# Kernel tuning notes

Hardware: AMD Instinct MI355X
Metric: run time of the kernel (lower is better)

## Reference

```python
import jax, jax.numpy as jnp
import numpy as np

B, S, V = 512, 256, 10      # batch, s_node_num, v_node_num
E, H = 128, 128             # embedding, lstm hidden
D = 2 * H                   # num_directions * hidden
PENALTY = 1.0e6
STD = 0.1


def _cell(x, h, c, Wih, Whh, b):
    # PyTorch LSTM cell, gate order i, f, g, o; b = b_ih + b_hh
    g = x @ Wih.T + h @ Whh.T + b
    i, f, gg, o = jnp.split(g, 4, axis=-1)
    c = jax.nn.sigmoid(f) * c + jax.nn.sigmoid(i) * jnp.tanh(gg)
    h = jax.nn.sigmoid(o) * jnp.tanh(c)
    return h, c


def setup_inputs() -> dict:
    key = jax.random.key(0)
    ks = jax.random.split(key, 25)
    w = lambda k, shp: (jax.random.normal(k, shp, jnp.float32) * STD)
    return {
        's_node_indexes': jax.random.randint(ks[0], (B, S), 0, S, dtype=jnp.int32),
        's_inputs': jax.random.uniform(ks[1], (B, S, 3), jnp.float32),
        'v_input': jax.random.uniform(ks[2], (V, 3), jnp.float32) * 0.5,
        'W_embed': w(ks[3], (E, 1)),
        'enc_Wih_f': w(ks[4], (4 * H, E)), 'enc_Whh_f': w(ks[5], (4 * H, H)), 'enc_b_f': w(ks[6], (4 * H,)),
        'enc_Wih_b': w(ks[7], (4 * H, E)), 'enc_Whh_b': w(ks[8], (4 * H, H)), 'enc_b_b': w(ks[9], (4 * H,)),
        'dec_Wih_f': w(ks[10], (4 * H, D)), 'dec_Whh_f': w(ks[11], (4 * H, H)), 'dec_b_f': w(ks[12], (4 * H,)),
        'dec_Wih_b': w(ks[13], (4 * H, D)), 'dec_Whh_b': w(ks[14], (4 * H, H)), 'dec_b_b': w(ks[15], (4 * H,)),
        'W_ref': w(ks[16], (D, D)), 'W_q': w(ks[17], (D, D)), 'v_w': w(ks[18], (D,)),
        'W_ref2': w(ks[19], (D, D)), 'W_q2': w(ks[20], (D, D)), 'v2_w': w(ks[21], (D,)),
    }


def reference(s_node_indexes, s_inputs, v_input, W_embed,
              enc_Wih_f, enc_Whh_f, enc_b_f, enc_Wih_b, enc_Whh_b, enc_b_b,
              dec_Wih_f, dec_Whh_f, dec_b_f, dec_Wih_b, dec_Whh_b, dec_b_b,
              W_ref, W_q, v_w, W_ref2, W_q2, v2_w):
    Bn, Sn = s_node_indexes.shape
    # Embed: snode resource -> Linear(1, E, bias=False)
    emb = s_inputs[:, :, 0:1] @ W_embed.T            # (B, S, E)
    xs = jnp.swapaxes(emb, 0, 1)                     # (S, B, E)
    h0 = jnp.zeros((Bn, H), jnp.float32)
    c0 = jnp.zeros((Bn, H), jnp.float32)

    def enc_scan(Wih, Whh, b, seq):
        def step(carry, x):
            h, c = carry
            h, c = _cell(x, h, c, Wih, Whh, b)
            return (h, c), h
        (hT, cT), hs = jax.lax.scan(step, (h0, c0), seq)
        return hs, hT, cT

    hs_f, hf, cf = enc_scan(enc_Wih_f, enc_Whh_f, enc_b_f, xs)
    hs_b, hb, cb = enc_scan(enc_Wih_b, enc_Whh_b, enc_b_b, xs[::-1])
    Enc = jnp.swapaxes(jnp.concatenate([hs_f, hs_b[::-1]], axis=-1), 0, 1)  # (B, S, D)
    h_state = jnp.stack([hf, hb])                    # (2, B, H)
    c_state = jnp.stack([cf, cb])

    refE = Enc @ W_ref.T                             # (B, S, D) precomputed (dropout p=0)
    ref2E = Enc @ W_ref2.T

    def dec_step(carry, vcpu):
        dec_in, h, c, played = carry                 # dec_in (B, D)
        hf_, cf_ = _cell(dec_in, h[0], c[0], dec_Wih_f, dec_Whh_f, dec_b_f)
        hb_, cb_ = _cell(dec_in, h[1], c[1], dec_Wih_b, dec_Whh_b, dec_b_b)
        dec_out = jnp.concatenate([hf_, hb_], axis=-1)                       # (B, D)
        cannot = (s_inputs[:, :, 0] < vcpu).astype(jnp.float32) + played     # (B, S)
        ow = jnp.tanh(refE + (dec_out @ W_q.T)[:, None, :]) @ v_w - PENALTY * cannot
        att = jax.nn.softmax(jnp.tanh(ref2E + (dec_in @ W_q2.T)[:, None, :]) @ v2_w, axis=1)
        new_in = jnp.einsum('bs,bsd->bd', att, Enc)
        sel = jnp.argmax(ow, axis=1)
        played = played + jax.nn.one_hot(sel, Sn, dtype=jnp.float32)
        return (new_in, jnp.stack([hf_, hb_]), jnp.stack([cf_, cb_]), played), (ow, sel)

    init = (jnp.zeros((Bn, D), jnp.float32), h_state, c_state, jnp.zeros((Bn, Sn), jnp.float32))
    _, (output_weights, sels) = jax.lax.scan(dec_step, init, v_input[:, 0])
    shuffled = sels.T                                # (B, V)
    original = jnp.take_along_axis(s_node_indexes, shuffled, axis=1)
    return original, shuffled, output_weights        # output_weights: (V, B, S)
```

## Files before the change

### kernel.cpp

```cpp
#include <hip/hip_runtime.h>
#include <math.h>

#define cB 512
#define cS 256
#define cV 10
#define cE 128
#define cH 128
#define cD 256
#define cG 512
#define PEN 1.0e6f
#define S1 224
#define PADK 40

typedef _Float16 half8_t __attribute__((ext_vector_type(8)));
typedef _Float16 half4_t __attribute__((ext_vector_type(4)));
typedef float f32x4 __attribute__((ext_vector_type(4)));

#define DOT4(acc, wv, hv)                                   \
    do {                                                    \
        acc = fmaf((wv).x, (hv).x, acc);                    \
        acc = fmaf((wv).y, (hv).y, acc);                    \
        acc = fmaf((wv).z, (hv).z, acc);                    \
        acc = fmaf((wv).w, (hv).w, acc);                    \
    } while (0)

__device__ __forceinline__ float sigmf(float x) { return 1.0f / (1.0f + expf(-x)); }

__global__ void k_uprep(const float* __restrict__ Wih_f, const float* __restrict__ Wih_b,
                        const float* __restrict__ W_embed, float* __restrict__ uvec)
{
    const int j = threadIdx.x;
    const float* __restrict__ Wih = blockIdx.x ? Wih_b : Wih_f;
    float u = 0.f;
#pragma unroll 8
    for (int e = 0; e < cE; ++e) u = fmaf(Wih[(size_t)j * cE + e], W_embed[e], u);
    uvec[blockIdx.x * cG + j] = u;
}

__global__ __launch_bounds__(1024, 4) void k_encoder(
    const float* __restrict__ s_inputs, const float* __restrict__ uvec,
    const float* __restrict__ Whh_f, const float* __restrict__ b_f,
    const float* __restrict__ Whh_b, const float* __restrict__ b_b,
    _Float16* __restrict__ Ehi, _Float16* __restrict__ Elo,
    float* __restrict__ h_state, float* __restrict__ c_state)
{
    const int dir = blockIdx.x >> 7;
    const int b0  = (blockIdx.x & 127) * 4;
    const float* __restrict__ Whh = dir ? Whh_b : Whh_f;
    const float* __restrict__ bv  = dir ? b_b   : b_f;
    const int tid = threadIdx.x;
    const int j = tid & 511;
    const int hf = tid >> 9;

    __shared__ __align__(16) float a_in[4][cS];
    __shared__ __align__(16) float hbuf[4][cH];
    __shared__ __align__(16) float gpart[4][2][516];

    a_in[tid >> 8][tid & 255] =
        s_inputs[((size_t)(b0 + (tid >> 8)) * cS + (tid & 255)) * 3];

    float4 w[16];
#pragma unroll
    for (int kk = 0; kk < 16; ++kk)
        w[kk] = *(const float4*)&Whh[(size_t)j * cH + hf * 64 + kk * 4];

    const float uj = (hf == 0) ? uvec[dir * cG + j] : 0.f;
    const float bj = (hf == 0) ? bv[j] : 0.f;

    const int ur = tid >> 7, uk = tid & 127;
    float c_reg = 0.f, h_last = 0.f;
    if (tid < 512) hbuf[ur][uk] = 0.f;
    __syncthreads();

    for (int p = 0; p < cS; ++p) {
        const int s = dir ? (cS - 1 - p) : p;
        float acc0 = fmaf(a_in[0][s], uj, bj);
        float acc1 = fmaf(a_in[1][s], uj, bj);
        float acc2 = fmaf(a_in[2][s], uj, bj);
        float acc3 = fmaf(a_in[3][s], uj, bj);
#pragma unroll
        for (int kk = 0; kk < 16; ++kk) {
            const float4 wv = w[kk];
            const float4 h0 = *(const float4*)&hbuf[0][hf * 64 + kk * 4];
            DOT4(acc0, wv, h0);
            const float4 h1 = *(const float4*)&hbuf[1][hf * 64 + kk * 4];
            DOT4(acc1, wv, h1);
            const float4 h2 = *(const float4*)&hbuf[2][hf * 64 + kk * 4];
            DOT4(acc2, wv, h2);
            const float4 h3 = *(const float4*)&hbuf[3][hf * 64 + kk * 4];
            DOT4(acc3, wv, h3);
        }
        gpart[0][hf][j] = acc0;
        gpart[1][hf][j] = acc1;
        gpart[2][hf][j] = acc2;
        gpart[3][hf][j] = acc3;
        __syncthreads();

        if (tid < 512) {
            const float gi = gpart[ur][0][uk]       + gpart[ur][1][uk];
            const float gf = gpart[ur][0][128 + uk] + gpart[ur][1][128 + uk];
            const float gg = gpart[ur][0][256 + uk] + gpart[ur][1][256 + uk];
            const float go = gpart[ur][0][384 + uk] + gpart[ur][1][384 + uk];
            const float i_ = sigmf(gi), f_ = sigmf(gf), g_ = tanhf(gg), o_ = sigmf(go);
            c_reg = fmaf(f_, c_reg, i_ * g_);
            const float hn = o_ * tanhf(c_reg);
            h_last = hn;
            hbuf[ur][uk] = hn;
            const size_t eidx = ((size_t)(b0 + ur) * cS + s) * cD + dir * cH + uk;
            const _Float16 hh = (_Float16)hn;
            Ehi[eidx] = hh;
            Elo[eidx] = (_Float16)(hn - (float)hh);
        }
        __syncthreads();
    }
    if (tid < 512) {
        h_state[((size_t)dir * cB + b0 + ur) * cH + uk] = h_last;
        c_state[((size_t)dir * cB + b0 + ur) * cH + uk] = c_reg;
    }
}

__global__ void k_split_w(const float* __restrict__ W1, const float* __restrict__ W2,
                          _Float16* __restrict__ Whi1, _Float16* __restrict__ Wlo1,
                          _Float16* __restrict__ Whi2, _Float16* __restrict__ Wlo2)
{
    const int i = blockIdx.x * 256 + threadIdx.x;
    {
        float a = W1[i]; _Float16 h = (_Float16)a;
        Whi1[i] = h; Wlo1[i] = (_Float16)(a - (float)h);
    }
    {
        float a = W2[i]; _Float16 h = (_Float16)a;
        Whi2[i] = h; Wlo2[i] = (_Float16)(a - (float)h);
    }
}

__global__ __launch_bounds__(256) void k_head_mat(
    const _Float16* __restrict__ Ahi, const _Float16* __restrict__ Alo,
    const _Float16* __restrict__ Whi, const _Float16* __restrict__ Wlo,
    float* __restrict__ outv)
{
    const int tid = threadIdx.x;
    const int w = tid >> 6, l = tid & 63;
    const int m0 = blockIdx.x * 64;

    __shared__ __align__(16) _Float16 As[2][64][PADK];
    __shared__ __align__(16) _Float16 Ws[2][256][PADK];

    const int r = tid >> 2, kq = tid & 3;
    size_t arow;
    {
        const int m = m0 + r;
        const int s = m >> 9, b = m & 511;
        arow = ((size_t)b * cS + s) * cD;
    }
    const size_t wrow = (size_t)tid * cD;

    f32x4 acc[16];
#pragma unroll
    for (int i = 0; i < 16; ++i) acc[i] = (f32x4){0.f, 0.f, 0.f, 0.f};

    const int fr = w * 16 + (l & 15);
    const int kc = (l >> 4) * 8;

    for (int k0 = 0; k0 < 256; k0 += 32) {
        __syncthreads();
        *(uint4*)&As[0][r][kq * 8] = *(const uint4*)&Ahi[arow + k0 + kq * 8];
        *(uint4*)&As[1][r][kq * 8] = *(const uint4*)&Alo[arow + k0 + kq * 8];
#pragma unroll
        for (int q4 = 0; q4 < 4; ++q4) {
            *(uint4*)&Ws[0][tid][q4 * 8] = *(const uint4*)&Whi[wrow + k0 + q4 * 8];
            *(uint4*)&Ws[1][tid][q4 * 8] = *(const uint4*)&Wlo[wrow + k0 + q4 * 8];
        }
        __syncthreads();

        const half8_t ahi = *(const half8_t*)&As[0][fr][kc];
        const half8_t alo = *(const half8_t*)&As[1][fr][kc];
#pragma unroll
        for (int nf = 0; nf < 16; ++nf) {
            const int n = nf * 16 + (l & 15);
            const half8_t bhi = *(const half8_t*)&Ws[0][n][kc];
            const half8_t blo = *(const half8_t*)&Ws[1][n][kc];
            acc[nf] = __builtin_amdgcn_mfma_f32_16x16x32_f16(ahi, bhi, acc[nf], 0, 0, 0);
            acc[nf] = __builtin_amdgcn_mfma_f32_16x16x32_f16(ahi, blo, acc[nf], 0, 0, 0);
            acc[nf] = __builtin_amdgcn_mfma_f32_16x16x32_f16(alo, bhi, acc[nf], 0, 0, 0);
        }
    }
#pragma unroll
    for (int nf = 0; nf < 16; ++nf)
#pragma unroll
        for (int rr = 0; rr < 4; ++rr) {
            const int m = w * 16 + ((l >> 4) << 2) + rr;
            outv[(size_t)(m0 + m) * cD + nf * 16 + (l & 15)] = acc[nf][rr];
        }
}

template <int MODE>
__global__ __launch_bounds__(512, 2) void k_head2(
    const _Float16* __restrict__ Ahi, const _Float16* __restrict__ Alo,
    const _Float16* __restrict__ Whi, const _Float16* __restrict__ Wlo,
    const float* __restrict__ qv, const float* __restrict__ vv,
    float* __restrict__ outv)
{
    const int tid = threadIdx.x;
    const int l = tid & 63;
    const int w = tid >> 6;
    const int wm = w >> 2, wn = w & 3;
    const int g = l >> 4, li = l & 15;
    const int m0 = blockIdx.x * 128;

    __shared__ __align__(16) _Float16 Ah[128][PADK];
    __shared__ __align__(16) _Float16 Al[128][PADK];
    __shared__ __align__(16) _Float16 Wh[256][PADK];
    __shared__ __align__(16) _Float16 Wl[256][PADK];
    __shared__ __align__(16) float qs[4][cD];
    __shared__ __align__(16) float vs[cD];
    __shared__ float spart[4][128];

    if (MODE == 0) {
        const int b = m0 >> 8;
        if (tid < 256) qs[0][tid] = qv[(size_t)b * cD + tid];
        else           vs[tid - 256] = vv[tid - 256];
    } else {
        const int b0 = m0 >> 5;
        qs[tid >> 8][tid & 255] = qv[(size_t)(b0 + (tid >> 8)) * cD + (tid & 255)];
        const int i2 = tid + 512;
        qs[i2 >> 8][i2 & 255] = qv[(size_t)(b0 + (i2 >> 8)) * cD + (i2 & 255)];
        if (tid < 256) vs[tid] = vv[tid];
    }

    const int ar = tid >> 2, aq = tid & 3;
    size_t arow;
    {
        const int m = m0 + ar;
        if (MODE == 0) arow = (size_t)m * cD;
        else { const int b = m >> 5, s = S1 + (m & 31); arow = ((size_t)b * cS + s) * cD; }
    }

    f32x4 acc[4][4];
#pragma unroll
    for (int mi = 0; mi < 4; ++mi)
#pragma unroll
        for (int ni = 0; ni < 4; ++ni) acc[mi][ni] = (f32x4){0.f, 0.f, 0.f, 0.f};

    for (int k0 = 0; k0 < 256; k0 += 32) {
        __syncthreads();
        *(uint4*)&Ah[ar][aq * 8] = *(const uint4*)&Ahi[arow + k0 + aq * 8];
        *(uint4*)&Al[ar][aq * 8] = *(const uint4*)&Alo[arow + k0 + aq * 8];
        *(uint4*)&Wh[ar][aq * 8] = *(const uint4*)&Whi[(size_t)ar * cD + k0 + aq * 8];
        *(uint4*)&Wl[ar][aq * 8] = *(const uint4*)&Wlo[(size_t)ar * cD + k0 + aq * 8];
        *(uint4*)&Wh[ar + 128][aq * 8] = *(const uint4*)&Whi[(size_t)(ar + 128) * cD + k0 + aq * 8];
        *(uint4*)&Wl[ar + 128][aq * 8] = *(const uint4*)&Wlo[(size_t)(ar + 128) * cD + k0 + aq * 8];
        __syncthreads();

        half8_t ah[4], al[4];
#pragma unroll
        for (int mi = 0; mi < 4; ++mi) {
            ah[mi] = *(const half8_t*)&Ah[wm * 64 + mi * 16 + li][g * 8];
            al[mi] = *(const half8_t*)&Al[wm * 64 + mi * 16 + li][g * 8];
        }
#pragma unroll
        for (int ni = 0; ni < 4; ++ni) {
            const half8_t bh = *(const half8_t*)&Wh[wn * 64 + ni * 16 + li][g * 8];
            const half8_t bl = *(const half8_t*)&Wl[wn * 64 + ni * 16 + li][g * 8];
#pragma unroll
            for (int mi = 0; mi < 4; ++mi) {
                acc[mi][ni] = __builtin_amdgcn_mfma_f32_16x16x32_f16(ah[mi], bh, acc[mi][ni], 0, 0, 0);
                acc[mi][ni] = __builtin_amdgcn_mfma_f32_16x16x32_f16(ah[mi], bl, acc[mi][ni], 0, 0, 0);
                acc[mi][ni] = __builtin_amdgcn_mfma_f32_16x16x32_f16(al[mi], bh, acc[mi][ni], 0, 0, 0);
            }
        }
    }

    float val = 0.f;
#pragma unroll
    for (int mi = 0; mi < 4; ++mi)
#pragma unroll
        for (int rr = 0; rr < 4; ++rr) {
            const int row = wm * 64 + mi * 16 + g * 4 + rr;
            const int bl = (MODE == 1) ? (row >> 5) : 0;
            float p = 0.f;
#pragma unroll
            for (int ni = 0; ni < 4; ++ni) {
                const int c = wn * 64 + ni * 16 + li;
                p = fmaf(vs[c], tanhf(acc[mi][ni][rr] + qs[bl][c]), p);
            }
            p += __shfl_xor(p, 1);
            p += __shfl_xor(p, 2);
            p += __shfl_xor(p, 4);
            p += __shfl_xor(p, 8);
            if (li == mi * 4 + rr) val = p;
        }
    {
        const int row_out = wm * 64 + (li >> 2) * 16 + g * 4 + (li & 3);
        spart[wn][row_out] = val;
    }
    __syncthreads();
    if (tid < 128)
        outv[m0 + tid] = spart[0][tid] + spart[1][tid] + spart[2][tid] + spart[3][tid];
}

__global__ __launch_bounds__(256, 4) void k_fold(
    const float* __restrict__ refC, const float* __restrict__ q1v,
    const float* __restrict__ v_w, float* __restrict__ sc1lo)
{
    const int tid = threadIdx.x;
    const int m0 = blockIdx.x * 64;
    const int r = tid >> 2, p = tid & 3;
    const int m = m0 + r;
    const int b = m & 511;
    __shared__ float red[64][4];

    const float* row  = refC + (size_t)m * cD + p * 64;
    const float* qrow = q1v + (size_t)b * cD + p * 64;
    const float* vrow = v_w + p * 64;
    float s = 0.f;
#pragma unroll 4
    for (int d = 0; d < 64; d += 4) {
        const float4 rv4 = *(const float4*)&row[d];
        const float4 q4  = *(const float4*)&qrow[d];
        const float4 v4  = *(const float4*)&vrow[d];
        s = fmaf(v4.x, tanhf(rv4.x + q4.x), s);
        s = fmaf(v4.y, tanhf(rv4.y + q4.y), s);
        s = fmaf(v4.z, tanhf(rv4.z + q4.z), s);
        s = fmaf(v4.w, tanhf(rv4.w + q4.w), s);
    }
    red[r][p] = s;
    __syncthreads();
    if (tid < 64)
        sc1lo[m0 + tid] = red[tid][0] + red[tid][1] + red[tid][2] + red[tid][3];
}

__global__ __launch_bounds__(512, 2) void k_dec_cells(
    const float* __restrict__ dec_in,
    const float* __restrict__ Wih_f, const float* __restrict__ Whh_f, const float* __restrict__ b_f,
    const float* __restrict__ Wih_b, const float* __restrict__ Whh_b, const float* __restrict__ b_b,
    float* __restrict__ h_state, float* __restrict__ c_state, float* __restrict__ dec_out)
{
    const int cell = blockIdx.x >> 7;
    const int b0 = (blockIdx.x & 127) * 4;
    const float* __restrict__ Wih = cell ? Wih_b : Wih_f;
    const float* __restrict__ Whh = cell ? Whh_b : Whh_f;
    const float* __restrict__ bv  = cell ? b_b   : b_f;
    const int j = threadIdx.x;

    __shared__ __align__(16) float xin[4][cD];
    __shared__ __align__(16) float hin[4][cH];
    __shared__ __align__(16) float gbuf[4][cG];

    for (int idx = j; idx < 4 * cD; idx += 512) {
        int bb = idx >> 8, k = idx & 255;
        xin[bb][k] = dec_in[(size_t)(b0 + bb) * cD + k];
    }
    {
        int bb = j >> 7, k = j & 127;
        hin[bb][k] = h_state[((size_t)cell * cB + b0 + bb) * cH + k];
    }
    __syncthreads();

    float a0 = bv[j];
    float a1 = a0, a2 = a0, a3 = a0;
#pragma unroll 4
    for (int kk = 0; kk < 64; ++kk) {
        const float4 wv = *(const float4*)&Wih[(size_t)j * cD + kk * 4];
        const float4 x0 = *(const float4*)&xin[0][kk * 4]; DOT4(a0, wv, x0);
        const float4 x1 = *(const float4*)&xin[1][kk * 4]; DOT4(a1, wv, x1);
        const float4 x2 = *(const float4*)&xin[2][kk * 4]; DOT4(a2, wv, x2);
        const float4 x3 = *(const float4*)&xin[3][kk * 4]; DOT4(a3, wv, x3);
    }
#pragma unroll 4
    for (int kk = 0; kk < 32; ++kk) {
        const float4 wv = *(const float4*)&Whh[(size_t)j * cH + kk * 4];
        const float4 h0 = *(const float4*)&hin[0][kk * 4]; DOT4(a0, wv, h0);
        const float4 h1 = *(const float4*)&hin[1][kk * 4]; DOT4(a1, wv, h1);
        const float4 h2 = *(const float4*)&hin[2][kk * 4]; DOT4(a2, wv, h2);
        const float4 h3 = *(const float4*)&hin[3][kk * 4]; DOT4(a3, wv, h3);
    }
    gbuf[0][j] = a0; gbuf[1][j] = a1; gbuf[2][j] = a2; gbuf[3][j] = a3;
    __syncthreads();

    const int uk = j & 127, ub = j >> 7;
    const float gi = gbuf[ub][uk];
    const float gf = gbuf[ub][128 + uk];
    const float gg = gbuf[ub][256 + uk];
    const float go = gbuf[ub][384 + uk];
    const size_t sidx = ((size_t)cell * cB + b0 + ub) * cH + uk;
    const float c_old = c_state[sidx];
    const float i_ = sigmf(gi), f_ = sigmf(gf), g_ = tanhf(gg), o_ = sigmf(go);
    const float cn = fmaf(f_, c_old, i_ * g_);
    const float hn = o_ * tanhf(cn);
    c_state[sidx] = cn;
    h_state[sidx] = hn;
    dec_out[(size_t)(b0 + ub) * cD + cell * cH + uk] = hn;
}

__global__ __launch_bounds__(256, 2) void k_qproj(
    const float* __restrict__ dec_out, const float* __restrict__ dec_in_old,
    const float* __restrict__ W_q, const float* __restrict__ W_q2,
    float* __restrict__ q1v, float* __restrict__ q2v)
{
    const int b = blockIdx.x;
    const int tid = threadIdx.x;
    __shared__ __align__(16) float dout[cD];
    __shared__ __align__(16) float din[cD];
    dout[tid] = dec_out[(size_t)b * cD + tid];
    din[tid]  = dec_in_old[(size_t)b * cD + tid];
    __syncthreads();
    float s1 = 0.0f, s2 = 0.0f;
#pragma unroll 4
    for (int kk = 0; kk < 64; ++kk) {
        const float4 w1 = *(const float4*)&W_q[(size_t)tid * cD + kk * 4];
        const float4 w2 = *(const float4*)&W_q2[(size_t)tid * cD + kk * 4];
        const float4 x1 = *(const float4*)&dout[kk * 4];
        const float4 x2 = *(const float4*)&din[kk * 4];
        DOT4(s1, w1, x1);
        DOT4(s2, w2, x2);
    }
    q1v[(size_t)b * cD + tid] = s1;
    q2v[(size_t)b * cD + tid] = s2;
}

__global__ __launch_bounds__(256, 2) void k_finish(
    const float* __restrict__ sc1lo, const float* __restrict__ sc1hi,
    const float* __restrict__ sc2,
    const _Float16* __restrict__ Ehi, const _Float16* __restrict__ Elo,
    const float* __restrict__ s_inputs, const int* __restrict__ s_node_indexes,
    const float* __restrict__ v_input, float* __restrict__ played,
    float* __restrict__ dec_in_new, float* __restrict__ outp, int t)
{
    const int b = blockIdx.x;
    const int tid = threadIdx.x;
    const int lane = tid & 63;
    const int wv = tid >> 6;

    __shared__ __align__(16) float atr[cS];
    __shared__ __align__(16) float part[4][cD];
    __shared__ float rv[cS];
    __shared__ int   ri[cS];

    const float owv = (tid < S1) ? sc1lo[(size_t)tid * cB + b]
                                 : sc1hi[(size_t)b * (cS - S1) + (tid - S1)];
    atr[tid] = sc2[(size_t)b * cS + tid];

    const float vcpu = v_input[t * 3];
    float val;
    {
        const float a0 = s_inputs[((size_t)b * cS + tid) * 3];
        const float can = (a0 < vcpu ? 1.0f : 0.0f) + played[(size_t)b * cS + tid];
        val = owv - PEN * can;
        outp[2 * cB * cV + ((size_t)t * cB + b) * cS + tid] = val;
    }
    rv[tid] = val; ri[tid] = tid;
    __syncthreads();
#pragma unroll
    for (int off = 128; off > 0; off >>= 1) {
        if (tid < off) {
            const float v2 = rv[tid + off]; const int i2 = ri[tid + off];
            const float v1 = rv[tid];       const int i1 = ri[tid];
            if (v2 > v1 || (v2 == v1 && i2 < i1)) { rv[tid] = v2; ri[tid] = i2; }
        }
        __syncthreads();
    }
    const int sel = ri[0];
    __syncthreads();
    if (tid == 0) {
        played[(size_t)b * cS + sel] += 1.0f;
        outp[(size_t)b * cV + t] = (float)s_node_indexes[(size_t)b * cS + sel];
        outp[(size_t)cB * cV + (size_t)b * cV + t] = (float)sel;
    }

    rv[tid] = atr[tid];
    __syncthreads();
#pragma unroll
    for (int off = 128; off > 0; off >>= 1) {
        if (tid < off) { const float v2 = rv[tid + off]; if (v2 > rv[tid]) rv[tid] = v2; }
        __syncthreads();
    }
    const float mx = rv[0];
    __syncthreads();
    const float ex = expf(atr[tid] - mx);
    rv[tid] = ex;
    __syncthreads();
#pragma unroll
    for (int off = 128; off > 0; off >>= 1) {
        if (tid < off) rv[tid] += rv[tid + off];
        __syncthreads();
    }
    const float ssum = rv[0];
    __syncthreads();
    atr[tid] = ex / ssum;
    __syncthreads();

    {
        float4 acc = make_float4(0.f, 0.f, 0.f, 0.f);
        for (int s2i = wv * 64; s2i < wv * 64 + 64; ++s2i) {
            const float a = atr[s2i];
            const size_t eidx = ((size_t)b * cS + s2i) * cD + lane * 4;
            const half4_t h4 = *(const half4_t*)&Ehi[eidx];
            const half4_t l4 = *(const half4_t*)&Elo[eidx];
            acc.x = fmaf(a, (float)h4[0] + (float)l4[0], acc.x);
            acc.y = fmaf(a, (float)h4[1] + (float)l4[1], acc.y);
            acc.z = fmaf(a, (float)h4[2] + (float)l4[2], acc.z);
            acc.w = fmaf(a, (float)h4[3] + (float)l4[3], acc.w);
        }
        *(float4*)&part[wv][lane * 4] = acc;
    }
    __syncthreads();
    dec_in_new[(size_t)b * cD + tid] =
        part[0][tid] + part[1][tid] + part[2][tid] + part[3][tid];
}

extern "C" void kernel_launch(void* const* d_in, const int* in_sizes, int n_in,
                              void* d_out, int out_size, void* d_ws, size_t ws_size,
                              hipStream_t stream)
{
    (void)in_sizes; (void)n_in; (void)out_size; (void)ws_size;

    const int*   s_node = (const int*)  d_in[0];
    const float* s_inp  = (const float*)d_in[1];
    const float* v_inp  = (const float*)d_in[2];
    const float* W_emb  = (const float*)d_in[3];
    const float* eWih_f = (const float*)d_in[4];
    const float* eWhh_f = (const float*)d_in[5];
    const float* eb_f   = (const float*)d_in[6];
    const float* eWih_b = (const float*)d_in[7];
    const float* eWhh_b = (const float*)d_in[8];
    const float* eb_b   = (const float*)d_in[9];
    const float* dWih_f = (const float*)d_in[10];
    const float* dWhh_f = (const float*)d_in[11];
    const float* db_f   = (const float*)d_in[12];
    const float* dWih_b = (const float*)d_in[13];
    const float* dWhh_b = (const float*)d_in[14];
    const float* db_b   = (const float*)d_in[15];
    const float* W_ref  = (const float*)d_in[16];
    const float* W_q    = (const float*)d_in[17];
    const float* v_w    = (const float*)d_in[18];
    const float* W_ref2 = (const float*)d_in[19];
    const float* W_q2   = (const float*)d_in[20];
    const float* v2_w   = (const float*)d_in[21];

    float* out = (float*)d_out;
    const size_t ENCSZ = (size_t)cB * cS * cD;
    const size_t SMALL = (size_t)cB * cD;

    char* p = (char*)d_ws;
    _Float16* Ehi = (_Float16*)p; p += ENCSZ * 2;
    _Float16* Elo = (_Float16*)p; p += ENCSZ * 2;
    float* refC  = (float*)p;     p += (size_t)S1 * cB * cD * 4;
    _Float16* Whi1 = (_Float16*)p; p += (size_t)cD * cD * 2;
    _Float16* Wlo1 = (_Float16*)p; p += (size_t)cD * cD * 2;
    _Float16* Whi2 = (_Float16*)p; p += (size_t)cD * cD * 2;
    _Float16* Wlo2 = (_Float16*)p; p += (size_t)cD * cD * 2;
    float* hst    = (float*)p; p += SMALL * 4;
    float* cst    = (float*)p; p += SMALL * 4;
    float* din0   = (float*)p; p += SMALL * 4;
    float* din1   = (float*)p; p += SMALL * 4;
    float* doutb  = (float*)p; p += SMALL * 4;
    float* played = (float*)p; p += SMALL * 4;
    float* q1v    = (float*)p; p += SMALL * 4;
    float* q2v    = (float*)p; p += SMALL * 4;
    float* sc2    = (float*)p; p += SMALL * 4;
    float* sc1lo  = (float*)p; p += (size_t)S1 * cB * 4;
    float* sc1hi  = (float*)p; p += (size_t)(cS - S1) * cB * 4;
    float* uvec   = (float*)p; p += 2 * cG * 4;

    hipMemsetAsync(played, 0, SMALL * sizeof(float), stream);
    hipMemsetAsync(din0,   0, SMALL * sizeof(float), stream);

    k_split_w<<<256, 256, 0, stream>>>(W_ref, W_ref2, Whi1, Wlo1, Whi2, Wlo2);
    k_uprep<<<2, 512, 0, stream>>>(eWih_f, eWih_b, W_emb, uvec);

    k_encoder<<<256, 1024, 0, stream>>>(s_inp, uvec, eWhh_f, eb_f, eWhh_b, eb_b,
                                        Ehi, Elo, hst, cst);

    k_head_mat<<<(S1 * cB) / 64, 256, 0, stream>>>(Ehi, Elo, Whi1, Wlo1, refC);

    for (int t = 0; t < cV; ++t) {
        float* di_old = (t & 1) ? din1 : din0;
        float* di_new = (t & 1) ? din0 : din1;
        k_dec_cells<<<256, 512, 0, stream>>>(di_old, dWih_f, dWhh_f, db_f,
                                             dWih_b, dWhh_b, db_b, hst, cst, doutb);
        k_qproj<<<512, 256, 0, stream>>>(doutb, di_old, W_q, W_q2, q1v, q2v);
        k_head2<0><<<(cB * cS) / 128, 512, 0, stream>>>(Ehi, Elo, Whi2, Wlo2,
                                                        q2v, v2_w, sc2);
        k_head2<1><<<(cB * (cS - S1)) / 128, 512, 0, stream>>>(Ehi, Elo, Whi1, Wlo1,
                                                               q1v, v_w, sc1hi);
        k_fold<<<(S1 * cB) / 64, 256, 0, stream>>>(refC, q1v, v_w, sc1lo);

        k_finish<<<512, 256, 0, stream>>>(sc1lo, sc1hi, sc2, Ehi, Elo,
                                          s_inp, s_node, v_inp, played, di_new, out, t);
    }
}
```

Baseline: 3.468 ms.

## Rebalance precomputed-vs-recomputed attention projections across both heads

Instead of caching W_ref·Enc for the first 224 positions and recomputing the rest plus the full W_ref2 projection every decoder step, both heads now cache part of their projection once (112 positions for the pointer head, 128 for the glimpse head). The remaining positions are recomputed per step with MFMA stripe kernels. The cached parts are folded with tanh/dot in one combined kernel. This trades per-step MFMA recompute of the attention head against extra fp32 cache traffic, and adds a second one-time projection GEMM plus more workspace. The encoder inner loop is also rewritten into unrolled array form with no change in behaviour.

```diff
diff --git a/kernel.cpp b/kernel.cpp
--- a/kernel.cpp
+++ b/kernel.cpp
@@ -9,8 +9,11 @@
 #define cD 256
 #define cG 512
 #define PEN 1.0e6f
-#define S1 224
 #define PADK 40
+#define S1OW 112
+#define L1OW 144
+#define S2AT 128
+#define L2AT 128
 
 typedef _Float16 half8_t __attribute__((ext_vector_type(8)));
 typedef _Float16 half4_t __attribute__((ext_vector_type(4)));
@@ -74,26 +77,20 @@
 
     for (int p = 0; p < cS; ++p) {
         const int s = dir ? (cS - 1 - p) : p;
-        float acc0 = fmaf(a_in[0][s], uj, bj);
-        float acc1 = fmaf(a_in[1][s], uj, bj);
-        float acc2 = fmaf(a_in[2][s], uj, bj);
-        float acc3 = fmaf(a_in[3][s], uj, bj);
+        float a0[4];
+#pragma unroll
+        for (int r = 0; r < 4; ++r) a0[r] = fmaf(a_in[r][s], uj, bj);
 #pragma unroll
         for (int kk = 0; kk < 16; ++kk) {
             const float4 wv = w[kk];
-            const float4 h0 = *(const float4*)&hbuf[0][hf * 64 + kk * 4];
-            DOT4(acc0, wv, h0);
-            const float4 h1 = *(const float4*)&hbuf[1][hf * 64 + kk * 4];
-            DOT4(acc1, wv, h1);
-            const float4 h2 = *(const float4*)&hbuf[2][hf * 64 + kk * 4];
-            DOT4(acc2, wv, h2);
-            const float4 h3 = *(const float4*)&hbuf[3][hf * 64 + kk * 4];
-            DOT4(acc3, wv, h3);
-        }
-        gpart[0][hf][j] = acc0;
-        gpart[1][hf][j] = acc1;
-        gpart[2][hf][j] = acc2;
-        gpart[3][hf][j] = acc3;
+#pragma unroll
+            for (int r = 0; r < 4; ++r) {
+                const float4 h4 = *(const float4*)&hbuf[r][hf * 64 + kk * 4];
+                DOT4(a0[r], wv, h4);
+            }
+        }
+#pragma unroll
+        for (int r = 0; r < 4; ++r) gpart[r][hf][j] = a0[r];
         __syncthreads();
 
         if (tid < 512) {
@@ -194,8 +191,96 @@
         }
 }
 
-template <int MODE>
-__global__ __launch_bounds__(512, 2) void k_head2(
+__global__ __launch_bounds__(512, 2) void k_stripe_att(
+    const _Float16* __restrict__ Ahi, const _Float16* __restrict__ Alo,
+    const _Float16* __restrict__ Whi, const _Float16* __restrict__ Wlo,
+    const float* __restrict__ qv, const float* __restrict__ vv,
+    float* __restrict__ outv)
+{
+    const int tid = threadIdx.x;
+    const int l = tid & 63;
+    const int w = tid >> 6;
+    const int wm = w >> 2, wn = w & 3;
+    const int g = l >> 4, li = l & 15;
+    const int b = blockIdx.x;
+
+    __shared__ __align__(16) _Float16 Ah[128][PADK];
+    __shared__ __align__(16) _Float16 Al[128][PADK];
+    __shared__ __align__(16) _Float16 Wh[256][PADK];
+    __shared__ __align__(16) _Float16 Wl[256][PADK];
+    __shared__ __align__(16) float qs[cD];
+    __shared__ __align__(16) float vs[cD];
+    __shared__ float spart[4][128];
+
+    if (tid < 256) qs[tid] = qv[(size_t)b * cD + tid];
+    else           vs[tid - 256] = vv[tid - 256];
+
+    const int ar = tid >> 2, aq = tid & 3;
+    const size_t arow = ((size_t)b * cS + S2AT + ar) * cD;
+
+    f32x4 acc[4][4];
+#pragma unroll
+    for (int mi = 0; mi < 4; ++mi)
+#pragma unroll
+        for (int ni = 0; ni < 4; ++ni) acc[mi][ni] = (f32x4){0.f, 0.f, 0.f, 0.f};
+
+    for (int k0 = 0; k0 < 256; k0 += 32) {
+        __syncthreads();
+        *(uint4*)&Ah[ar][aq * 8] = *(const uint4*)&Ahi[arow + k0 + aq * 8];
+        *(uint4*)&Al[ar][aq * 8] = *(const uint4*)&Alo[arow + k0 + aq * 8];
+        *(uint4*)&Wh[ar][aq * 8] = *(const uint4*)&Whi[(size_t)ar * cD + k0 + aq * 8];
+        *(uint4*)&Wl[ar][aq * 8] = *(const uint4*)&Wlo[(size_t)ar * cD + k0 + aq * 8];
+        *(uint4*)&Wh[ar + 128][aq * 8] = *(const uint4*)&Whi[(size_t)(ar + 128) * cD + k0 + aq * 8];
+        *(uint4*)&Wl[ar + 128][aq * 8] = *(const uint4*)&Wlo[(size_t)(ar + 128) * cD + k0 + aq * 8];
+        __syncthreads();
+
+        half8_t ah[4], al[4];
+#pragma unroll
+        for (int mi = 0; mi < 4; ++mi) {
+            ah[mi] = *(const half8_t*)&Ah[wm * 64 + mi * 16 + li][g * 8];
+            al[mi] = *(const half8_t*)&Al[wm * 64 + mi * 16 + li][g * 8];
+        }
+#pragma unroll
+        for (int ni = 0; ni < 4; ++ni) {
+            const half8_t bh = *(const half8_t*)&Wh[wn * 64 + ni * 16 + li][g * 8];
+            const half8_t bl = *(const half8_t*)&Wl[wn * 64 + ni * 16 + li][g * 8];
+#pragma unroll
+            for (int mi = 0; mi < 4; ++mi) {
+                acc[mi][ni] = __builtin_amdgcn_mfma_f32_16x16x32_f16(ah[mi], bh, acc[mi][ni], 0, 0, 0);
+                acc[mi][ni] = __builtin_amdgcn_mfma_f32_16x16x32_f16(ah[mi], bl, acc[mi][ni], 0, 0, 0);
+                acc[mi][ni] = __builtin_amdgcn_mfma_f32_16x16x32_f16(al[mi], bh, acc[mi][ni], 0, 0, 0);
+            }
+        }
+    }
+
+    float val = 0.f;
+#pragma unroll
+    for (int mi = 0; mi < 4; ++mi)
+#pragma unroll
+        for (int rr = 0; rr < 4; ++rr) {
+            float p = 0.f;
+#pragma unroll
+            for (int ni = 0; ni < 4; ++ni) {
+                const int c = wn * 64 + ni * 16 + li;
+                p = fmaf(vs[c], tanhf(acc[mi][ni][rr] + qs[c]), p);
+            }
+            p += __shfl_xor(p, 1);
+            p += __shfl_xor(p, 2);
+            p += __shfl_xor(p, 4);
+            p += __shfl_xor(p, 8);
+            if (li == mi * 4 + rr) val = p;
+        }
+    {
+        const int row_out = wm * 64 + (li >> 2) * 16 + g * 4 + (li & 3);
+        spart[wn][row_out] = val;
+    }
+    __syncthreads();
+    if (tid < 128)
+        outv[(size_t)b * L2AT + tid] =
+            spart[0][tid] + spart[1][tid] + spart[2][tid] + spart[3][tid];
+}
+
+__global__ __launch_bounds__(512, 2) void k_stripe_ow(
     const _Float16* __restrict__ Ahi, const _Float16* __restrict__ Alo,
     const _Float16* __restrict__ Whi, const _Float16* __restrict__ Wlo,
     const float* __restrict__ qv, const float* __restrict__ vv,
@@ -212,28 +297,18 @@
     __shared__ __align__(16) _Float16 Al[128][PADK];
     __shared__ __align__(16) _Float16 Wh[256][PADK];
     __shared__ __align__(16) _Float16 Wl[256][PADK];
-    __shared__ __align__(16) float qs[4][cD];
     __shared__ __align__(16) float vs[cD];
     __shared__ float spart[4][128];
 
-    if (MODE == 0) {
-        const int b = m0 >> 8;
-        if (tid < 256) qs[0][tid] = qv[(size_t)b * cD + tid];
-        else           vs[tid - 256] = vv[tid - 256];
-    } else {
-        const int b0 = m0 >> 5;
-        qs[tid >> 8][tid & 255] = qv[(size_t)(b0 + (tid >> 8)) * cD + (tid & 255)];
-        const int i2 = tid + 512;
-        qs[i2 >> 8][i2 & 255] = qv[(size_t)(b0 + (i2 >> 8)) * cD + (i2 & 255)];
-        if (tid < 256) vs[tid] = vv[tid];
-    }
+    if (tid < 256) vs[tid] = vv[tid];
 
     const int ar = tid >> 2, aq = tid & 3;
     size_t arow;
     {
         const int m = m0 + ar;
-        if (MODE == 0) arow = (size_t)m * cD;
-        else { const int b = m >> 5, s = S1 + (m & 31); arow = ((size_t)b * cS + s) * cD; }
+        const int bq = m / L1OW;
+        const int s = S1OW + (m - bq * L1OW);
+        arow = ((size_t)bq * cS + s) * cD;
     }
 
     f32x4 acc[4][4];
@@ -277,12 +352,12 @@
 #pragma unroll
         for (int rr = 0; rr < 4; ++rr) {
             const int row = wm * 64 + mi * 16 + g * 4 + rr;
-            const int bl = (MODE == 1) ? (row >> 5) : 0;
+            const int bq = (m0 + row) / L1OW;
             float p = 0.f;
 #pragma unroll
             for (int ni = 0; ni < 4; ++ni) {
                 const int c = wn * 64 + ni * 16 + li;
-                p = fmaf(vs[c], tanhf(acc[mi][ni][rr] + qs[bl][c]), p);
+                p = fmaf(vs[c], tanhf(acc[mi][ni][rr] + qv[(size_t)bq * cD + c]), p);
             }
             p += __shfl_xor(p, 1);
             p += __shfl_xor(p, 2);
@@ -296,38 +371,8 @@
     }
     __syncthreads();
     if (tid < 128)
-        outv[m0 + tid] = spart[0][tid] + spart[1][tid] + spart[2][tid] + spart[3][tid];
-}
-
-__global__ __launch_bounds__(256, 4) void k_fold(
-    const float* __restrict__ refC, const float* __restrict__ q1v,
-    const float* __restrict__ v_w, float* __restrict__ sc1lo)
-{
-    const int tid = threadIdx.x;
-    const int m0 = blockIdx.x * 64;
-    const int r = tid >> 2, p = tid & 3;
-    const int m = m0 + r;
-    const int b = m & 511;
-    __shared__ float red[64][4];
-
-    const float* row  = refC + (size_t)m * cD + p * 64;
-    const float* qrow = q1v + (size_t)b * cD + p * 64;
-    const float* vrow = v_w + p * 64;
-    float s = 0.f;
-#pragma unroll 4
-    for (int d = 0; d < 64; d += 4) {
-        const float4 rv4 = *(const float4*)&row[d];
-        const float4 q4  = *(const float4*)&qrow[d];
-        const float4 v4  = *(const float4*)&vrow[d];
-        s = fmaf(v4.x, tanhf(rv4.x + q4.x), s);
-        s = fmaf(v4.y, tanhf(rv4.y + q4.y), s);
-        s = fmaf(v4.z, tanhf(rv4.z + q4.z), s);
-        s = fmaf(v4.w, tanhf(rv4.w + q4.w), s);
-    }
-    red[r][p] = s;
-    __syncthreads();
-    if (tid < 64)
-        sc1lo[m0 + tid] = red[tid][0] + red[tid][1] + red[tid][2] + red[tid][3];
+        outv[m0 + tid] =
+            spart[0][tid] + spart[1][tid] + spart[2][tid] + spart[3][tid];
 }
 
 __global__ __launch_bounds__(512, 2) void k_dec_cells(
@@ -419,9 +464,49 @@
     q2v[(size_t)b * cD + tid] = s2;
 }
 
+__global__ __launch_bounds__(256, 4) void k_dualfold(
+    const float* __restrict__ refC, const float* __restrict__ ref2C,
+    const float* __restrict__ q1v, const float* __restrict__ q2v,
+    const float* __restrict__ v_w, const float* __restrict__ v2_w,
+    float* __restrict__ sc1lo, float* __restrict__ sc2lo)
+{
+    const int tid = threadIdx.x;
+    const int blk = blockIdx.x;
+    const bool isow = blk < (S1OW * cB / 64);
+    const float* __restrict__ C  = isow ? refC : ref2C;
+    const float* __restrict__ qv = isow ? q1v : q2v;
+    const float* __restrict__ vv = isow ? v_w : v2_w;
+    float* __restrict__ outv     = isow ? sc1lo : sc2lo;
+    const int m0 = (isow ? blk : blk - S1OW * cB / 64) * 64;
+
+    const int r = tid >> 2, p = tid & 3;
+    const int m = m0 + r;
+    const int b = m & 511;
+    __shared__ float red[64][4];
+
+    const float* row  = C + (size_t)m * cD + p * 64;
+    const float* qrow = qv + (size_t)b * cD + p * 64;
+    const float* vrow = vv + p * 64;
+    float s = 0.f;
+#pragma unroll 4
+    for (int d = 0; d < 64; d += 4) {
+        const float4 rv4 = *(const float4*)&row[d];
+        const float4 q4  = *(const float4*)&qrow[d];
+        const float4 v4  = *(const float4*)&vrow[d];
+        s = fmaf(v4.x, tanhf(rv4.x + q4.x), s);
+        s = fmaf(v4.y, tanhf(rv4.y + q4.y), s);
+        s = fmaf(v4.z, tanhf(rv4.z + q4.z), s);
+        s = fmaf(v4.w, tanhf(rv4.w + q4.w), s);
+    }
+    red[r][p] = s;
+    __syncthreads();
+    if (tid < 64)
+        outv[m0 + tid] = red[tid][0] + red[tid][1] + red[tid][2] + red[tid][3];
+}
+
 __global__ __launch_bounds__(256, 2) void k_finish(
     const float* __restrict__ sc1lo, const float* __restrict__ sc1hi,
-    const float* __restrict__ sc2,
+    const float* __restrict__ sc2lo, const float* __restrict__ sc2hi,
     const _Float16* __restrict__ Ehi, const _Float16* __restrict__ Elo,
     const float* __restrict__ s_inputs, const int* __restrict__ s_node_indexes,
     const float* __restrict__ v_input, float* __restrict__ played,
@@ -437,9 +522,10 @@
     __shared__ float rv[cS];
     __shared__ int   ri[cS];
 
-    const float owv = (tid < S1) ? sc1lo[(size_t)tid * cB + b]
-                                 : sc1hi[(size_t)b * (cS - S1) + (tid - S1)];
-    atr[tid] = sc2[(size_t)b * cS + tid];
+    const float owv = (tid < S1OW) ? sc1lo[(size_t)tid * cB + b]
+                                   : sc1hi[(size_t)b * L1OW + (tid - S1OW)];
+    atr[tid] = (tid < S2AT) ? sc2lo[(size_t)tid * cB + b]
+                            : sc2hi[(size_t)b * L2AT + (tid - S2AT)];
 
     const float vcpu = v_input[t * 3];
     float val;
@@ -543,9 +629,10 @@
     const size_t SMALL = (size_t)cB * cD;
 
     char* p = (char*)d_ws;
-    _Float16* Ehi = (_Float16*)p; p += ENCSZ * 2;
-    _Float16* Elo = (_Float16*)p; p += ENCSZ * 2;
-    float* refC  = (float*)p;     p += (size_t)S1 * cB * cD * 4;
+    _Float16* Ehi  = (_Float16*)p; p += ENCSZ * 2;
+    _Float16* Elo  = (_Float16*)p; p += ENCSZ * 2;
+    float* refC    = (float*)p;    p += (size_t)S1OW * cB * cD * 4;
+    float* ref2C   = (float*)p;    p += (size_t)S2AT * cB * cD * 4;
     _Float16* Whi1 = (_Float16*)p; p += (size_t)cD * cD * 2;
     _Float16* Wlo1 = (_Float16*)p; p += (size_t)cD * cD * 2;
     _Float16* Whi2 = (_Float16*)p; p += (size_t)cD * cD * 2;
@@ -558,9 +645,10 @@
     float* played = (float*)p; p += SMALL * 4;
     float* q1v    = (float*)p; p += SMALL * 4;
     float* q2v    = (float*)p; p += SMALL * 4;
-    float* sc2    = (float*)p; p += SMALL * 4;
-    float* sc1lo  = (float*)p; p += (size_t)S1 * cB * 4;
-    float* sc1hi  = (float*)p; p += (size_t)(cS - S1) * cB * 4;
+    float* sc1lo  = (float*)p; p += (size_t)S1OW * cB * 4;
+    float* sc1hi  = (float*)p; p += (size_t)L1OW * cB * 4;
+    float* sc2lo  = (float*)p; p += (size_t)S2AT * cB * 4;
+    float* sc2hi  = (float*)p; p += (size_t)L2AT * cB * 4;
     float* uvec   = (float*)p; p += 2 * cG * 4;
 
     hipMemsetAsync(played, 0, SMALL * sizeof(float), stream);
@@ -572,7 +660,8 @@
     k_encoder<<<256, 1024, 0, stream>>>(s_inp, uvec, eWhh_f, eb_f, eWhh_b, eb_b,
                                         Ehi, Elo, hst, cst);
 
-    k_head_mat<<<(S1 * cB) / 64, 256, 0, stream>>>(Ehi, Elo, Whi1, Wlo1, refC);
+    k_head_mat<<<(S1OW * cB) / 64, 256, 0, stream>>>(Ehi, Elo, Whi1, Wlo1, refC);
+    k_head_mat<<<(S2AT * cB) / 64, 256, 0, stream>>>(Ehi, Elo, Whi2, Wlo2, ref2C);
 
     for (int t = 0; t < cV; ++t) {
         float* di_old = (t & 1) ? din1 : din0;
@@ -580,13 +669,13 @@
         k_dec_cells<<<256, 512, 0, stream>>>(di_old, dWih_f, dWhh_f, db_f,
                                              dWih_b, dWhh_b, db_b, hst, cst, doutb);
         k_qproj<<<512, 256, 0, stream>>>(doutb, di_old, W_q, W_q2, q1v, q2v);
-        k_head2<0><<<(cB * cS) / 128, 512, 0, stream>>>(Ehi, Elo, Whi2, Wlo2,
-                                                        q2v, v2_w, sc2);
-        k_head2<1><<<(cB * (cS - S1)) / 128, 512, 0, stream>>>(Ehi, Elo, Whi1, Wlo1,
-                                                               q1v, v_w, sc1hi);
-        k_fold<<<(S1 * cB) / 64, 256, 0, stream>>>(refC, q1v, v_w, sc1lo);
-
-        k_finish<<<512, 256, 0, stream>>>(sc1lo, sc1hi, sc2, Ehi, Elo,
+        k_stripe_ow<<<(cB * L1OW) / 128, 512, 0, stream>>>(Ehi, Elo, Whi1, Wlo1,
+                                                           q1v, v_w, sc1hi);
+        k_stripe_att<<<cB, 512, 0, stream>>>(Ehi, Elo, Whi2, Wlo2,
+                                             q2v, v2_w, sc2hi);
+        k_dualfold<<<((S1OW + S2AT) * cB) / 64, 256, 0, stream>>>(
+            refC, ref2C, q1v, q2v, v_w, v2_w, sc1lo, sc2lo);
+        k_finish<<<512, 256, 0, stream>>>(sc1lo, sc1hi, sc2lo, sc2hi, Ehi, Elo,
                                           s_inp, s_node, v_inp, played, di_new, out, t);
     }
 }
```

Result: slower. 3.784 ms (+9.1%).
